# Performance work log

Measured on AMD Instinct MI355X. Metric: run time of the kernel, lower is better.

## Reference

```python
import jax, jax.numpy as jnp
import numpy as np

K = 3          # kernel size
PAD = 1
K2 = K * K
G = 4          # groups (conv groups == offset groups)
EPS = 1e-5


def _conv2d(x, w, b):
    # x: [N,C,H,W], w: [O,I,kh,kw], stride 1, pad 1
    y = jax.lax.conv_general_dilated(
        x, w, window_strides=(1, 1), padding=((PAD, PAD), (PAD, PAD)),
        dimension_numbers=("NCHW", "OIHW", "NCHW"))
    return y + b[None, :, None, None]


def _deform_conv(x2d, offset, conv_w, conv_b):
    # x2d: [N,C,H,W]; offset: [N, 2*G*K2, H, W] (layout: 2*(g*K2+k)+{0:y,1:x})
    N, C, H, W = x2d.shape
    Cg = C // G
    Cout = conv_w.shape[0]
    Og = Cout // G

    off = offset.reshape(N, G, K2, 2, H, W)
    off_y = off[:, :, :, 0]          # [N,G,K2,H,W]
    off_x = off[:, :, :, 1]

    kk = jnp.arange(K, dtype=offset.dtype) - PAD            # [-1,0,1]
    ky2 = jnp.repeat(kk, K)                                  # k = kh*K + kw
    kx2 = jnp.tile(kk, K)
    base_y = jnp.arange(H, dtype=offset.dtype)[None, :] + ky2[:, None]  # [K2,H]
    base_x = jnp.arange(W, dtype=offset.dtype)[None, :] + kx2[:, None]  # [K2,W]

    py = off_y + base_y[None, None, :, :, None]   # [N,G,K2,H,W]
    px = off_x + base_x[None, None, :, None, :]

    y0f = jnp.floor(py); x0f = jnp.floor(px)
    ly = py - y0f; lx = px - x0f
    y0 = y0f.astype(jnp.int32); x0 = x0f.astype(jnp.int32)
    y1 = y0 + 1; x1 = x0 + 1

    # channels-last grouped view for gathers: [N,G,H,W,Cg]
    xg = x2d.reshape(N, G, Cg, H, W).transpose(0, 1, 3, 4, 2)
    nI = jnp.arange(N)[:, None, None, None, None]
    gI = jnp.arange(G)[None, :, None, None, None]

    def corner(yi, xi):
        valid = (yi >= 0) & (yi < H) & (xi >= 0) & (xi < W)
        yc = jnp.clip(yi, 0, H - 1)
        xc = jnp.clip(xi, 0, W - 1)
        v = xg[nI, gI, yc, xc]                    # [N,G,K2,H,W,Cg]
        return v * valid[..., None].astype(x2d.dtype)

    w00 = ((1 - ly) * (1 - lx))[..., None]
    w01 = ((1 - ly) * lx)[..., None]
    w10 = (ly * (1 - lx))[..., None]
    w11 = (ly * lx)[..., None]
    sampled = (w00 * corner(y0, x0) + w01 * corner(y0, x1)
               + w10 * corner(y1, x0) + w11 * corner(y1, x1))  # [N,G,K2,H,W,Cg]

    wG = conv_w.reshape(G, Og, Cg, K2)
    out = jnp.einsum('ngkhwc,gock->ngohw', sampled, wG)         # [N,G,Og,H,W]
    out = out.reshape(N, Cout, H, W) + conv_b[None, :, None, None]
    return out


def setup_inputs() -> dict:
    key = jax.random.key(0)
    ks = jax.random.split(key, 5)
    B, C, D, H, W = 2, 128, 6, 56, 56
    Cout = 128
    x = jax.random.normal(ks[0], (B, C, D, H, W), dtype=jnp.float32)
    # offset conv: small init so sampling displacements stay modest
    offset_w = jax.random.normal(ks[1], (2 * G * K2, C, K, K), dtype=jnp.float32) * 0.01
    offset_b = jnp.zeros((2 * G * K2,), dtype=jnp.float32)
    fan_in = (C // G) * K2
    conv_w = jax.random.normal(ks[2], (Cout, C // G, K, K), dtype=jnp.float32) / np.sqrt(fan_in)
    conv_b = jax.random.normal(ks[3], (Cout,), dtype=jnp.float32) * 0.01
    return {"x": x, "offset_w": offset_w, "offset_b": offset_b,
            "conv_w": conv_w, "conv_b": conv_b}


def reference(x, offset_w, offset_b, conv_w, conv_b):
    B, C, D, H, W = x.shape
    x2d = x.transpose(0, 2, 1, 3, 4).reshape(B * D, C, H, W)
    offset = _conv2d(x2d, offset_w, offset_b)
    out = _deform_conv(x2d, offset, conv_w, conv_b)           # [B*D, Cout, H, W]
    Cout = out.shape[1]
    out = out.reshape(B, D, Cout, H, W).transpose(0, 2, 1, 3, 4)  # [B,Cout,D,H,W]
    # instance norm: per (b, c) over (D, H, W), no affine
    mu = jnp.mean(out, axis=(2, 3, 4), keepdims=True)
    var = jnp.var(out, axis=(2, 3, 4), keepdims=True)
    out = (out - mu) * jax.lax.rsqrt(var + EPS)
    # exact GELU
    return 0.5 * out * (1.0 + jax.lax.erf(out / jnp.sqrt(2.0).astype(out.dtype)))
```

## Files before the change

kernel.cpp:

```cpp
#include <hip/hip_runtime.h>
#include <hip/hip_bf16.h>

typedef __attribute__((ext_vector_type(8))) short bf16x8;
typedef __attribute__((ext_vector_type(4))) float f32x4;

#define B_   2
#define C_   128
#define D_   6
#define H_   56
#define W_   56
#define N_   12
#define HW   3136
#define CSTR (D_*HW)
#define COUT 128
#define OFFP 80

__device__ __forceinline__ float bf2f(ushort u) {
  return __uint_as_float(((unsigned int)u) << 16);
}
__device__ __forceinline__ ushort f2bf(float f) {
  unsigned int x = __float_as_uint(f);
  x += 0x7FFFu + ((x >> 16) & 1u);
  return (ushort)(x >> 16);
}

__global__ __launch_bounds__(256) void k_transpose(const float* __restrict__ x,
                                                   ushort* __restrict__ xcl) {
  __shared__ float tile[32][57];
  const int h = blockIdx.x, c0 = blockIdx.y * 32, n = blockIdx.z;
  const int b = n / D_, d = n % D_;
  const float* src = x + (((size_t)(b * C_ + c0) * D_ + d) * HW) + h * W_;
  for (int i = threadIdx.x; i < 32 * W_; i += 256) {
    const int c = i / W_, w = i - c * W_;
    tile[c][w] = src[(size_t)c * CSTR + w];
  }
  __syncthreads();
  ushort* dst = xcl + ((size_t)(n * HW + h * W_)) * C_ + c0;
  for (int i = threadIdx.x; i < 32 * W_; i += 256) {
    const int w = i >> 5, c = i & 31;
    dst[(size_t)w * C_ + c] = f2bf(tile[c][w]);
  }
}

__global__ void k_wprep(const float* __restrict__ cw, const float* __restrict__ ow,
                        ushort* __restrict__ wd2, ushort* __restrict__ wob2) {
  const int idx = blockIdx.x * 256 + threadIdx.x;
  if (idx < COUT * 288) {
    const int g = idx / 9216;
    const int r = idx - g * 9216;
    const int kb = r >> 8;
    const int co_l = (r >> 3) & 31;
    const int e = r & 7;
    const int ts = kb >> 2;
    const int q = kb & 3;
    wd2[idx] = f2bf(cw[((size_t)(g * 32 + co_l) * 32 + q * 8 + e) * 9 + ts]);
  } else if (idx < COUT * 288 + 144 * OFFP * 8) {
    const int i2 = idx - COUT * 288;
    const int e = i2 & 7;
    const int co = (i2 >> 3) % OFFP;
    const int kb = i2 / (OFFP * 8);
    const int tap = kb >> 4;
    const int r16 = kb & 15;
    const int kq = r16 >> 2;
    const int q = r16 & 3;
    const int c = kq * 32 + q * 8 + e;
    float v = 0.f;
    if (co < 72) v = ow[((size_t)co * C_ + c) * 9 + tap];
    wob2[i2] = f2bf(v);
  }
}

__global__ __launch_bounds__(320) void k_offset_conv(const ushort* __restrict__ xcl,
    const ushort* __restrict__ wob2, const float* __restrict__ ob,
    float* __restrict__ offb2) {
  __shared__ __align__(16) ushort xr[3 * 24 * 128];
  const int w0 = blockIdx.x * 16;
  const int h = blockIdx.y, n = blockIdx.z;
  const int t = threadIdx.x;
  for (int i = t; i < 864; i += 320) {
    const int c16 = i & 15;
    const int sdy = i >> 4;
    const int s = sdy % 18;
    const int dy = sdy / 18;
    const int w = w0 - 1 + s;
    const int rr = h + dy - 1;
    const int c0 = c16 * 8;
    const int db = (((dy * 24 + s) * 128 + c0) * 2) ^ ((s & 7) << 4);
    uint4 v = {0u, 0u, 0u, 0u};
    if ((unsigned)rr < (unsigned)H_ && (unsigned)w < (unsigned)W_)
      v = *(const uint4*)(xcl + ((size_t)(n * HW + rr * W_ + w)) * C_ + c0);
    *(uint4*)((char*)xr + db) = v;
  }
  __syncthreads();
  const int l = t & 63;
  const int nt = t >> 6;
  const int lf = l & 15, q = l >> 4;
  const ushort* wbase = wob2 + ((size_t)q * OFFP + nt * 16 + lf) * 8;
  f32x4 acc = {};
  bf16x8 Bf[9][4];
#pragma unroll
  for (int kq = 0; kq < 4; ++kq)
    Bf[0][kq] = *(const bf16x8*)(wbase + (size_t)(kq * 4) * OFFP * 8);
#pragma unroll
  for (int tap = 0; tap < 9; ++tap) {
    if (tap < 8) {
#pragma unroll
      for (int kq = 0; kq < 4; ++kq)
        Bf[tap + 1][kq] = *(const bf16x8*)(wbase +
            (size_t)((tap + 1) * 16 + kq * 4) * OFFP * 8);
    }
    const int dy = tap / 3, kxr = tap - dy * 3;
    const int s = lf + kxr;
#pragma unroll
    for (int kq = 0; kq < 4; ++kq) {
      const int ab = (((dy * 24 + s) * 128 + kq * 32 + q * 8) * 2) ^ ((s & 7) << 4);
      const bf16x8 a = *(const bf16x8*)((const char*)xr + ab);
      acc = __builtin_amdgcn_mfma_f32_16x16x32_bf16(a, Bf[tap][kq], acc, 0, 0, 0);
    }
  }
  const int co = nt * 16 + lf;
  const float bias = (co < 72) ? ob[co] : 0.f;
  float* orow = offb2 + ((size_t)n * HW + h * W_) * OFFP;
#pragma unroll
  for (int r = 0; r < 4; ++r) {
    const int w = w0 + q * 4 + r;
    if (w < W_) orow[(size_t)w * OFFP + co] = acc[r] + bias;
  }
}

__global__ __launch_bounds__(256) void k_deform(const ushort* __restrict__ xcl,
    const float* __restrict__ offb2, const ushort* __restrict__ wd2,
    const float* __restrict__ cb, float* __restrict__ out) {
  __shared__ __align__(16) unsigned char sm[14208];
  __shared__ __align__(16) float outs[2560];
  ushort* swW = (ushort*)sm;
  int* swO = (int*)(sm + 4736);

  const int hw0 = blockIdx.x * 16;
  const int n = blockIdx.y;
  const int t = threadIdx.x;

  for (int i = t; i < 576; i += 256) {
    const int p = i / 36;
    const int r = i - p * 36;
    const int g = r / 9;
    const int k = r - g * 9;
    const int hw = hw0 + p;
    const int h = hw / 56;
    const int w = hw - h * 56;
    const float2 o2 = *(const float2*)(offb2 + (size_t)(n * HW + hw) * OFFP + g * 18 + 2 * k);
    const int ky = k / 3 - 1;
    const int kx = k - (k / 3) * 3 - 1;
    const float py = (float)(h + ky) + o2.x;
    const float px = (float)(w + kx) + o2.y;
    const float y0f = floorf(py), x0f = floorf(px);
    const float ly = py - y0f, lx = px - x0f;
    const int y0 = (int)y0f, x0 = (int)x0f;
    const int y1 = y0 + 1, x1 = x0 + 1;
    const int yc0 = min(max(y0, 0), H_ - 1), yc1 = min(max(y1, 0), H_ - 1);
    const int xc0 = min(max(x0, 0), W_ - 1), xc1 = min(max(x1, 0), W_ - 1);
    const float my0 = ((unsigned)y0 < (unsigned)H_) ? 1.f : 0.f;
    const float my1 = ((unsigned)y1 < (unsigned)H_) ? 1.f : 0.f;
    const float mx0 = ((unsigned)x0 < (unsigned)W_) ? 1.f : 0.f;
    const float mx1 = ((unsigned)x1 < (unsigned)W_) ? 1.f : 0.f;
    ushort4 wq;
    wq.x = f2bf((1.f - ly) * (1.f - lx) * my0 * mx0);
    wq.y = f2bf((1.f - ly) * lx * my0 * mx1);
    wq.z = f2bf(ly * (1.f - lx) * my1 * mx0);
    wq.w = f2bf(ly * lx * my1 * mx1);
    *(ushort4*)(swW + p * 148 + (g * 9 + k) * 4) = wq;
    int4 oq;
    oq.x = (yc0 * 56 + xc0) * 128;
    oq.y = (yc0 * 56 + xc1) * 128;
    oq.z = (yc1 * 56 + xc0) * 128;
    oq.w = (yc1 * 56 + xc1) * 128;
    *(int4*)(swO + p * 148 + (g * 9 + k) * 4) = oq;
  }
  __syncthreads();

  const int l = t & 63;
  const int g = t >> 6;
  const int lf = l & 15, q = l >> 4;
  const ushort* xb = xcl + (size_t)n * HW * C_ + g * 32 + q * 8;
  const ushort* bb = wd2 + ((size_t)(g * 36 + q) * 32 + lf) * 8;
  const int sbase = lf * 148 + g * 36;
  f32x4 acc0 = {}, acc1 = {};

  ushort4 wq[9]; int4 oq[9];
  uint4 A00[9], A01[9], A10[9], A11[9];
  bf16x8 B0[9], B1[9];

#define LOADT(s_) do { \
    wq[s_] = *(const ushort4*)(swW + sbase + (s_) * 4); \
    oq[s_] = *(const int4*)(swO + sbase + (s_) * 4); } while (0)
#define GATHER(s_) do { \
    A00[s_] = *(const uint4*)(xb + oq[s_].x); \
    A01[s_] = *(const uint4*)(xb + oq[s_].y); \
    A10[s_] = *(const uint4*)(xb + oq[s_].z); \
    A11[s_] = *(const uint4*)(xb + oq[s_].w); } while (0)
#define LOADB(s_) do { \
    B0[s_] = *(const bf16x8*)(bb + (size_t)(s_) * 1024); \
    B1[s_] = *(const bf16x8*)(bb + (size_t)(s_) * 1024 + 128); } while (0)

  LOADT(0); LOADT(1);
  GATHER(0); LOADB(0);
#pragma unroll
  for (int ts = 0; ts < 9; ++ts) {
    if (ts < 7) LOADT(ts + 2);
    if (ts < 8) { GATHER(ts + 1); LOADB(ts + 1); }
    const float w00 = bf2f(wq[ts].x), w01 = bf2f(wq[ts].y);
    const float w10 = bf2f(wq[ts].z), w11 = bf2f(wq[ts].w);
    bf16x8 av;
#pragma unroll
    for (int j = 0; j < 4; ++j) {
      const unsigned int u00 = ((const unsigned int*)&A00[ts])[j];
      const unsigned int u01 = ((const unsigned int*)&A01[ts])[j];
      const unsigned int u10 = ((const unsigned int*)&A10[ts])[j];
      const unsigned int u11 = ((const unsigned int*)&A11[ts])[j];
      const float lo = fmaf(w00, __uint_as_float(u00 << 16),
                       fmaf(w01, __uint_as_float(u01 << 16),
                       fmaf(w10, __uint_as_float(u10 << 16),
                            w11 * __uint_as_float(u11 << 16))));
      const float hi = fmaf(w00, __uint_as_float(u00 & 0xFFFF0000u),
                       fmaf(w01, __uint_as_float(u01 & 0xFFFF0000u),
                       fmaf(w10, __uint_as_float(u10 & 0xFFFF0000u),
                            w11 * __uint_as_float(u11 & 0xFFFF0000u))));
      av[2 * j]     = (short)f2bf(lo);
      av[2 * j + 1] = (short)f2bf(hi);
    }
    acc0 = __builtin_amdgcn_mfma_f32_16x16x32_bf16(av, B0[ts], acc0, 0, 0, 0);
    acc1 = __builtin_amdgcn_mfma_f32_16x16x32_bf16(av, B1[ts], acc1, 0, 0, 0);
  }
#undef LOADT
#undef GATHER
#undef LOADB

#pragma unroll
  for (int r = 0; r < 4; ++r) {
    outs[(g * 32 + lf) * 20 + q * 4 + r] = acc0[r] + cb[g * 32 + lf];
    outs[(g * 32 + 16 + lf) * 20 + q * 4 + r] = acc1[r] + cb[g * 32 + 16 + lf];
  }
  __syncthreads();
  {
    const int co = t & 127;
    const int hf = t >> 7;
    const float4 v0 = *(const float4*)(outs + co * 20 + hf * 8);
    const float4 v1 = *(const float4*)(outs + co * 20 + hf * 8 + 4);
    const int b = n / D_, d = n - b * D_;
    float* dst = out + ((size_t)(b * COUT + co) * D_ + d) * HW + hw0 + hf * 8;
    *(float4*)dst = v0;
    *(float4*)(dst + 4) = v1;
  }
}

__global__ __launch_bounds__(1024) void k_norm_gelu(float* __restrict__ io) {
  const int M = D_ * HW;
  const int M4 = M / 4;
  float4* p = (float4*)(io + (size_t)blockIdx.x * M);
  float s = 0.f, s2 = 0.f;
  for (int i = threadIdx.x; i < M4; i += 1024) {
    const float4 v = p[i];
    s += v.x + v.y + v.z + v.w;
    s2 = fmaf(v.x, v.x, fmaf(v.y, v.y, fmaf(v.z, v.z, fmaf(v.w, v.w, s2))));
  }
#pragma unroll
  for (int off = 32; off > 0; off >>= 1) {
    s += __shfl_down(s, off, 64);
    s2 += __shfl_down(s2, off, 64);
  }
  __shared__ float rs[16], rs2[16];
  __shared__ float smu, srstd;
  const int wid = threadIdx.x >> 6, lane = threadIdx.x & 63;
  if (lane == 0) { rs[wid] = s; rs2[wid] = s2; }
  __syncthreads();
  if (threadIdx.x == 0) {
    float ts = 0.f, t2 = 0.f;
#pragma unroll
    for (int i = 0; i < 16; ++i) { ts += rs[i]; t2 += rs2[i]; }
    const float mu = ts / (float)M;
    const float var = t2 / (float)M - mu * mu;
    smu = mu;
    srstd = rsqrtf(var + 1e-5f);
  }
  __syncthreads();
  const float mu = smu, rstd = srstd;
  for (int i = threadIdx.x; i < M4; i += 1024) {
    float4 v = p[i];
    v.x = (v.x - mu) * rstd; v.y = (v.y - mu) * rstd;
    v.z = (v.z - mu) * rstd; v.w = (v.w - mu) * rstd;
    v.x = 0.5f * v.x * (1.f + erff(v.x * 0.70710678118654752f));
    v.y = 0.5f * v.y * (1.f + erff(v.y * 0.70710678118654752f));
    v.z = 0.5f * v.z * (1.f + erff(v.z * 0.70710678118654752f));
    v.w = 0.5f * v.w * (1.f + erff(v.w * 0.70710678118654752f));
    p[i] = v;
  }
}

extern "C" void kernel_launch(void* const* d_in, const int* in_sizes, int n_in,
                              void* d_out, int out_size, void* d_ws, size_t ws_size,
                              hipStream_t stream) {
  const float* x  = (const float*)d_in[0];
  const float* ow = (const float*)d_in[1];
  const float* ob = (const float*)d_in[2];
  const float* cw = (const float*)d_in[3];
  const float* cb = (const float*)d_in[4];
  float* outp = (float*)d_out;

  char* wsb = (char*)d_ws;
  ushort* xcl   = (ushort*)wsb;
  float*  offb2 = (float*)(wsb + 9633792);
  ushort* wd2   = (ushort*)(wsb + 21676032);
  ushort* wob2  = (ushort*)(wsb + 21749760);

  k_wprep<<<dim3(504), 256, 0, stream>>>(cw, ow, wd2, wob2);
  k_transpose<<<dim3(H_, 4, N_), 256, 0, stream>>>(x, xcl);
  k_offset_conv<<<dim3(4, H_, N_), 320, 0, stream>>>(xcl, wob2, ob, offb2);
  k_deform<<<dim3(196, N_), 256, 0, stream>>>(xcl, offb2, wd2, cb, outp);
  k_norm_gelu<<<dim3(B_ * COUT), 1024, 0, stream>>>(outp);
}
```

Baseline: 164.8 us.

## Process 32 pixels per deform block to reuse weight fragments across two tiles

Each deform-conv block now covers 32 output pixels instead of 16. Every wave computes two 16-pixel M-tiles, so the B (conv weight) fragments loaded per tap are reused by two MFMA pairs, and the grid is halved. The output staging buffer now aliases the sampling-table shared memory, guarded by an extra barrier, and the row pitch is changed to 33 to avoid bank conflicts. The per-tap prefetch is simplified to one stage and a sched_barrier is added. This doubles the gather registers held per thread, which risks lower occupancy or spills, and the smaller grid gives less parallelism.

```diff
diff --git a/kernel.cpp b/kernel.cpp
--- a/kernel.cpp
+++ b/kernel.cpp
@@ -131,16 +131,16 @@
 __global__ __launch_bounds__(256) void k_deform(const ushort* __restrict__ xcl,
     const float* __restrict__ offb2, const ushort* __restrict__ wd2,
     const float* __restrict__ cb, float* __restrict__ out) {
-  __shared__ __align__(16) unsigned char sm[14208];
-  __shared__ __align__(16) float outs[2560];
+  __shared__ __align__(16) unsigned char sm[28416];
   ushort* swW = (ushort*)sm;
-  int* swO = (int*)(sm + 4736);
-
-  const int hw0 = blockIdx.x * 16;
+  int* swO = (int*)(sm + 9472);
+  float* outs = (float*)sm;
+
+  const int hw0 = blockIdx.x * 32;
   const int n = blockIdx.y;
   const int t = threadIdx.x;
 
-  for (int i = t; i < 576; i += 256) {
+  for (int i = t; i < 1152; i += 256) {
     const int p = i / 36;
     const int r = i - p * 36;
     const int g = r / 9;
@@ -168,13 +168,13 @@
     wq.y = f2bf((1.f - ly) * lx * my0 * mx1);
     wq.z = f2bf(ly * (1.f - lx) * my1 * mx0);
     wq.w = f2bf(ly * lx * my1 * mx1);
-    *(ushort4*)(swW + p * 148 + (g * 9 + k) * 4) = wq;
+    *(ushort4*)(swW + (p * 37 + g * 9 + k) * 4) = wq;
     int4 oq;
     oq.x = (yc0 * 56 + xc0) * 128;
     oq.y = (yc0 * 56 + xc1) * 128;
     oq.z = (yc1 * 56 + xc0) * 128;
     oq.w = (yc1 * 56 + xc1) * 128;
-    *(int4*)(swO + p * 148 + (g * 9 + k) * 4) = oq;
+    *(int4*)(swO + (p * 37 + g * 9 + k) * 4) = oq;
   }
   __syncthreads();
 
@@ -183,73 +183,92 @@
   const int lf = l & 15, q = l >> 4;
   const ushort* xb = xcl + (size_t)n * HW * C_ + g * 32 + q * 8;
   const ushort* bb = wd2 + ((size_t)(g * 36 + q) * 32 + lf) * 8;
-  const int sbase = lf * 148 + g * 36;
-  f32x4 acc0 = {}, acc1 = {};
-
-  ushort4 wq[9]; int4 oq[9];
-  uint4 A00[9], A01[9], A10[9], A11[9];
+  const int sb0 = (lf * 37 + g * 9) * 4;
+  const int sb1 = ((lf + 16) * 37 + g * 9) * 4;
+  f32x4 acc00 = {}, acc01 = {}, acc10 = {}, acc11 = {};
+
+  ushort4 wq0[9], wq1[9]; int4 oq0[9], oq1[9];
+  uint4 A0a[9], A0b[9], A0c[9], A0d[9];
+  uint4 A1a[9], A1b[9], A1c[9], A1d[9];
   bf16x8 B0[9], B1[9];
 
-#define LOADT(s_) do { \
-    wq[s_] = *(const ushort4*)(swW + sbase + (s_) * 4); \
-    oq[s_] = *(const int4*)(swO + sbase + (s_) * 4); } while (0)
-#define GATHER(s_) do { \
-    A00[s_] = *(const uint4*)(xb + oq[s_].x); \
-    A01[s_] = *(const uint4*)(xb + oq[s_].y); \
-    A10[s_] = *(const uint4*)(xb + oq[s_].z); \
-    A11[s_] = *(const uint4*)(xb + oq[s_].w); } while (0)
-#define LOADB(s_) do { \
+#define PREF(s_) do { \
+    wq0[s_] = *(const ushort4*)(swW + sb0 + (s_) * 4); \
+    oq0[s_] = *(const int4*)(swO + sb0 + (s_) * 4); \
+    wq1[s_] = *(const ushort4*)(swW + sb1 + (s_) * 4); \
+    oq1[s_] = *(const int4*)(swO + sb1 + (s_) * 4); \
+    A0a[s_] = *(const uint4*)(xb + oq0[s_].x); \
+    A0b[s_] = *(const uint4*)(xb + oq0[s_].y); \
+    A0c[s_] = *(const uint4*)(xb + oq0[s_].z); \
+    A0d[s_] = *(const uint4*)(xb + oq0[s_].w); \
+    A1a[s_] = *(const uint4*)(xb + oq1[s_].x); \
+    A1b[s_] = *(const uint4*)(xb + oq1[s_].y); \
+    A1c[s_] = *(const uint4*)(xb + oq1[s_].z); \
+    A1d[s_] = *(const uint4*)(xb + oq1[s_].w); \
     B0[s_] = *(const bf16x8*)(bb + (size_t)(s_) * 1024); \
     B1[s_] = *(const bf16x8*)(bb + (size_t)(s_) * 1024 + 128); } while (0)
 
-  LOADT(0); LOADT(1);
-  GATHER(0); LOADB(0);
+#define LERP(av_, wqv_, Aa_, Ab_, Ac_, Ad_) do { \
+    const float w00 = bf2f(wqv_.x), w01 = bf2f(wqv_.y); \
+    const float w10 = bf2f(wqv_.z), w11 = bf2f(wqv_.w); \
+    _Pragma("unroll") \
+    for (int j = 0; j < 4; ++j) { \
+      const unsigned int u00 = ((const unsigned int*)&Aa_)[j]; \
+      const unsigned int u01 = ((const unsigned int*)&Ab_)[j]; \
+      const unsigned int u10 = ((const unsigned int*)&Ac_)[j]; \
+      const unsigned int u11 = ((const unsigned int*)&Ad_)[j]; \
+      const float lo = fmaf(w00, __uint_as_float(u00 << 16), \
+                       fmaf(w01, __uint_as_float(u01 << 16), \
+                       fmaf(w10, __uint_as_float(u10 << 16), \
+                            w11 * __uint_as_float(u11 << 16)))); \
+      const float hi = fmaf(w00, __uint_as_float(u00 & 0xFFFF0000u), \
+                       fmaf(w01, __uint_as_float(u01 & 0xFFFF0000u), \
+                       fmaf(w10, __uint_as_float(u10 & 0xFFFF0000u), \
+                            w11 * __uint_as_float(u11 & 0xFFFF0000u)))); \
+      av_[2 * j]     = (short)f2bf(lo); \
+      av_[2 * j + 1] = (short)f2bf(hi); \
+    } } while (0)
+
+  PREF(0);
 #pragma unroll
   for (int ts = 0; ts < 9; ++ts) {
-    if (ts < 7) LOADT(ts + 2);
-    if (ts < 8) { GATHER(ts + 1); LOADB(ts + 1); }
-    const float w00 = bf2f(wq[ts].x), w01 = bf2f(wq[ts].y);
-    const float w10 = bf2f(wq[ts].z), w11 = bf2f(wq[ts].w);
-    bf16x8 av;
-#pragma unroll
-    for (int j = 0; j < 4; ++j) {
-      const unsigned int u00 = ((const unsigned int*)&A00[ts])[j];
-      const unsigned int u01 = ((const unsigned int*)&A01[ts])[j];
-      const unsigned int u10 = ((const unsigned int*)&A10[ts])[j];
-      const unsigned int u11 = ((const unsigned int*)&A11[ts])[j];
-      const float lo = fmaf(w00, __uint_as_float(u00 << 16),
-                       fmaf(w01, __uint_as_float(u01 << 16),
-                       fmaf(w10, __uint_as_float(u10 << 16),
-                            w11 * __uint_as_float(u11 << 16))));
-      const float hi = fmaf(w00, __uint_as_float(u00 & 0xFFFF0000u),
-                       fmaf(w01, __uint_as_float(u01 & 0xFFFF0000u),
-                       fmaf(w10, __uint_as_float(u10 & 0xFFFF0000u),
-                            w11 * __uint_as_float(u11 & 0xFFFF0000u))));
-      av[2 * j]     = (short)f2bf(lo);
-      av[2 * j + 1] = (short)f2bf(hi);
+    if (ts < 8) PREF(ts + 1);
+    __builtin_amdgcn_sched_barrier(0);
+    {
+      bf16x8 av0, av1;
+      LERP(av0, wq0[ts], A0a[ts], A0b[ts], A0c[ts], A0d[ts]);
+      acc00 = __builtin_amdgcn_mfma_f32_16x16x32_bf16(av0, B0[ts], acc00, 0, 0, 0);
+      acc01 = __builtin_amdgcn_mfma_f32_16x16x32_bf16(av0, B1[ts], acc01, 0, 0, 0);
+      LERP(av1, wq1[ts], A1a[ts], A1b[ts], A1c[ts], A1d[ts]);
+      acc10 = __builtin_amdgcn_mfma_f32_16x16x32_bf16(av1, B0[ts], acc10, 0, 0, 0);
+      acc11 = __builtin_amdgcn_mfma_f32_16x16x32_bf16(av1, B1[ts], acc11, 0, 0, 0);
     }
-    acc0 = __builtin_amdgcn_mfma_f32_16x16x32_bf16(av, B0[ts], acc0, 0, 0, 0);
-    acc1 = __builtin_amdgcn_mfma_f32_16x16x32_bf16(av, B1[ts], acc1, 0, 0, 0);
-  }
-#undef LOADT
-#undef GATHER
-#undef LOADB
-
-#pragma unroll
-  for (int r = 0; r < 4; ++r) {
-    outs[(g * 32 + lf) * 20 + q * 4 + r] = acc0[r] + cb[g * 32 + lf];
-    outs[(g * 32 + 16 + lf) * 20 + q * 4 + r] = acc1[r] + cb[g * 32 + 16 + lf];
+  }
+#undef PREF
+#undef LERP
+
+  __syncthreads();
+  {
+    const float b0 = cb[g * 32 + lf];
+    const float b1 = cb[g * 32 + 16 + lf];
+#pragma unroll
+    for (int r = 0; r < 4; ++r) {
+      outs[(g * 32 + lf) * 33 + q * 4 + r]       = acc00[r] + b0;
+      outs[(g * 32 + 16 + lf) * 33 + q * 4 + r]  = acc01[r] + b1;
+      outs[(g * 32 + lf) * 33 + 16 + q * 4 + r]      = acc10[r] + b0;
+      outs[(g * 32 + 16 + lf) * 33 + 16 + q * 4 + r] = acc11[r] + b1;
+    }
   }
   __syncthreads();
   {
     const int co = t & 127;
     const int hf = t >> 7;
-    const float4 v0 = *(const float4*)(outs + co * 20 + hf * 8);
-    const float4 v1 = *(const float4*)(outs + co * 20 + hf * 8 + 4);
+    const float* srcp = outs + co * 33 + hf * 16;
     const int b = n / D_, d = n - b * D_;
-    float* dst = out + ((size_t)(b * COUT + co) * D_ + d) * HW + hw0 + hf * 8;
-    *(float4*)dst = v0;
-    *(float4*)(dst + 4) = v1;
+    float* dst = out + ((size_t)(b * COUT + co) * D_ + d) * HW + hw0 + hf * 16;
+#pragma unroll
+    for (int v4 = 0; v4 < 4; ++v4)
+      *(float4*)(dst + v4 * 4) = *(const float4*)(srcp + v4 * 4);
   }
 }
 
@@ -315,6 +334,6 @@
   k_wprep<<<dim3(504), 256, 0, stream>>>(cw, ow, wd2, wob2);
   k_transpose<<<dim3(H_, 4, N_), 256, 0, stream>>>(x, xcl);
   k_offset_conv<<<dim3(4, H_, N_), 320, 0, stream>>>(xcl, wob2, ob, offb2);
-  k_deform<<<dim3(196, N_), 256, 0, stream>>>(xcl, offb2, wd2, cb, outp);
+  k_deform<<<dim3(98, N_), 256, 0, stream>>>(xcl, offb2, wd2, cb, outp);
   k_norm_gelu<<<dim3(B_ * COUT), 1024, 0, stream>>>(outp);
 }
```

After: 164.8 us. Within noise of the previous version (-0.0%).
